# Optimization experiments

Measured on AMD Instinct MI355X. Metric: run time of the kernel, lower is better.

Reference implementation:

```python
import jax, jax.numpy as jnp
import numpy as np

B, T, N, D = 4, 12, 512, 128
L = 4            # max_lag + 1 lag encoders
H = D // 2       # lag-encoder hidden dim
THRESHOLD = 0.1


def setup_inputs() -> dict:
    key = jax.random.key(0)
    ks = jax.random.split(key, 10)
    s = 0.02
    return {
        "x":   jax.random.normal(ks[0], (B, T, N, D), dtype=jnp.float32),
        # lag encoders: Linear(D->H), ReLU, Linear(H->D), stacked over L lags
        "W1":  s * jax.random.normal(ks[1], (L, D, H), dtype=jnp.float32),
        "b1":  jnp.zeros((L, H), dtype=jnp.float32),
        "W2":  s * jax.random.normal(ks[2], (L, H, D), dtype=jnp.float32),
        "b2":  jnp.zeros((L, D), dtype=jnp.float32),
        # causal scorer: Linear(2D->D), ReLU, (Dropout=id in eval), Linear(D->1), Sigmoid
        "Ws1": s * jax.random.normal(ks[3], (2 * D, D), dtype=jnp.float32),
        "bs1": jnp.zeros((D,), dtype=jnp.float32),
        "Ws2": s * jax.random.normal(ks[4], (D, 1), dtype=jnp.float32),
        "bs2": jnp.zeros((1,), dtype=jnp.float32),
    }


def reference(x, W1, b1, W2, b2, Ws1, bs1, Ws2, bs2):
    Tdim = x.shape[1]
    # lagged slices x[:, T-1-lag] for lag in 0..L-1 (all lags active since T > max_lag)
    lags = jnp.stack([x[:, max(0, Tdim - 1 - l)] for l in range(L)], axis=1)  # (B,L,N,D)
    h = jax.nn.relu(jnp.einsum('blnd,ldh->blnh', lags, W1) + b1[None, :, None, :])
    enc = jnp.einsum('blnh,lhd->blnd', h, W2) + b2[None, :, None, :]          # (B,L,N,D)
    agg = enc.mean(axis=1)                                                    # (B,N,D)

    # pairwise causal scorer. cat([src, tgt]) @ Ws1 == src @ Ws1[:D] + tgt @ Ws1[D:],
    # avoiding the explicit (B,N,N,2D) concat.
    src_proj = jnp.einsum('bnd,dk->bnk', agg, Ws1[:D])   # (B,N,D)
    tgt_proj = jnp.einsum('bnd,dk->bnk', agg, Ws1[D:])   # (B,N,D)
    pre = src_proj[:, :, None, :] + tgt_proj[:, None, :, :] + bs1  # (B,N,N,D)
    score = jax.nn.sigmoid(jnp.einsum('bijd,d->bij', jax.nn.relu(pre), Ws2[:, 0]) + bs2[0])

    # threshold sparsification + remove self loops
    adj = jnp.where(score > THRESHOLD, score, 0.0)
    adj = adj * (1.0 - jnp.eye(N, dtype=adj.dtype))

    # multi-hop propagation and global max normalization per batch element
    a2 = jnp.matmul(adj, adj)
    a3 = jnp.matmul(a2, adj)
    enhanced = adj + 0.5 * a2 + 0.25 * a3
    mx = jnp.max(enhanced, axis=(-1, -2), keepdims=True)
    return enhanced / (mx + 1e-8)
```

## Files before the change

kernel.cpp:

```cpp
#include <hip/hip_runtime.h>
#include <math.h>

#define Bn 4
#define Tn 12
#define Nn 512
#define Dn 128
#define Ln 4
#define Hn 64

typedef __attribute__((ext_vector_type(8))) short short8;
typedef __attribute__((ext_vector_type(4))) float f32x4;
typedef _Float16 h2 __attribute__((ext_vector_type(2)));

__device__ __forceinline__ unsigned short f2bf(float f) {
    unsigned int u = __float_as_uint(f);
    unsigned int r = (u + 0x7FFF + ((u >> 16) & 1)) >> 16;
    return (unsigned short)r;
}
__device__ __forceinline__ float bf2f(unsigned short s) {
    return __uint_as_float(((unsigned int)s) << 16);
}
__device__ __forceinline__ float fdot2(h2 a, h2 b, float c) {
#if defined(__has_builtin)
#if __has_builtin(__builtin_amdgcn_fdot2)
    return __builtin_amdgcn_fdot2(a, b, c, false);
#else
    return c + (float)a.x*(float)b.x + (float)a.y*(float)b.y;
#endif
#else
    return c + (float)a.x*(float)b.x + (float)a.y*(float)b.y;
#endif
}

__global__ __launch_bounds__(256) void k_prep(
    const float* __restrict__ W1, const float* __restrict__ W2, const float* __restrict__ Ws1,
    unsigned short* __restrict__ w1p, unsigned short* __restrict__ w2p,
    unsigned short* __restrict__ wsp)
{
    int g = blockIdx.x*256 + threadIdx.x;
    unsigned short tmp[8];
    if (g < 4096) {
        int lag = g >> 10, r = g & 1023;
        int n = r >> 4, k8 = r & 15;
        #pragma unroll
        for (int j = 0; j < 8; ++j) tmp[j] = f2bf(W1[(size_t)(lag*128 + k8*8 + j)*64 + n]);
        *(short8*)(w1p + (size_t)lag*8192 + n*128 + k8*8) = *(const short8*)tmp;
    } else if (g < 8192) {
        int r = g - 4096;
        int n = r >> 5, k8 = r & 31;
        #pragma unroll
        for (int j = 0; j < 8; ++j) tmp[j] = f2bf(W2[(size_t)(k8*8 + j)*128 + n]);
        *(short8*)(w2p + (size_t)n*256 + k8*8) = *(const short8*)tmp;
    } else {
        int r = g - 8192;
        int tgt = r >> 11, r2 = r & 2047;
        int n = r2 >> 4, k8 = r2 & 15;
        #pragma unroll
        for (int j = 0; j < 8; ++j) tmp[j] = f2bf(Ws1[(size_t)(tgt*128 + k8*8 + j)*128 + n]);
        *(short8*)(wsp + (size_t)tgt*16384 + n*128 + k8*8) = *(const short8*)tmp;
    }
}

__global__ __launch_bounds__(256) void k_enc(
    const float* __restrict__ x,  const float* __restrict__ b1,
    const float* __restrict__ b2, const float* __restrict__ bs1,
    const unsigned short* __restrict__ w1p, const unsigned short* __restrict__ w2p,
    const unsigned short* __restrict__ wsp,
    unsigned short* __restrict__ spb, unsigned short* __restrict__ tpb,
    unsigned int* __restrict__ maxslot)
{
    __shared__ __align__(16) unsigned short hA[16*264];
    __shared__ __align__(16) unsigned short xA[16*136];
    __shared__ __align__(16) unsigned short aggA[16*136];
    int tid  = threadIdx.x;
    int bid  = blockIdx.x;
    int wv   = __builtin_amdgcn_readfirstlane(tid >> 6);
    int lane = tid & 63;
    if (bid == 0 && tid < Bn) maxslot[tid] = 0u;

    int r0 = bid * 16;
    int bb = r0 >> 9, n0 = r0 & 511;
    int m = lane & 15, q = lane >> 4;
    int colL = lane & 15, rq = lane >> 4;

    for (int lag = 0; lag < Ln; ++lag) {
        __syncthreads();
        {
            const float4* xs = (const float4*)(x + ((size_t)(bb*Tn + (Tn-1-lag))*Nn + n0)*Dn);
            for (int v = tid; v < 512; v += 256) {
                float4 f = xs[v];
                int row = v >> 5, c4 = v & 31;
                ushort4 o = { f2bf(f.x), f2bf(f.y), f2bf(f.z), f2bf(f.w) };
                *(ushort4*)&xA[row*136 + c4*4] = o;
            }
        }
        __syncthreads();
        f32x4 acc = {0.f,0.f,0.f,0.f};
        #pragma unroll
        for (int ks = 0; ks < 4; ++ks) {
            short8 af = *(const short8*)&xA[m*136 + ks*32 + q*8];
            short8 bg = *(const short8*)(w1p + (size_t)lag*8192 + (wv*16+m)*128 + ks*32 + q*8);
            acc = __builtin_amdgcn_mfma_f32_16x16x32_bf16(af, bg, acc, 0, 0, 0);
        }
        int ncol = wv*16 + colL;
        float bv = b1[lag*Hn + ncol];
        #pragma unroll
        for (int reg = 0; reg < 4; ++reg)
            hA[(rq*4+reg)*264 + lag*64 + ncol] = f2bf(fmaxf(acc[reg] + bv, 0.f));
    }
    __syncthreads();

    #pragma unroll
    for (int ch = 0; ch < 2; ++ch) {
        f32x4 acc = {0.f,0.f,0.f,0.f};
        #pragma unroll
        for (int ks = 0; ks < 8; ++ks) {
            short8 af = *(const short8*)&hA[m*264 + ks*32 + q*8];
            short8 bg = *(const short8*)(w2p + (size_t)(ch*64 + wv*16 + m)*256 + ks*32 + q*8);
            acc = __builtin_amdgcn_mfma_f32_16x16x32_bf16(af, bg, acc, 0, 0, 0);
        }
        int col = ch*64 + wv*16 + colL;
        float b2s = b2[col] + b2[Dn+col] + b2[2*Dn+col] + b2[3*Dn+col];
        #pragma unroll
        for (int reg = 0; reg < 4; ++reg)
            aggA[(rq*4+reg)*136 + col] = f2bf(0.25f*(acc[reg] + b2s));
    }
    __syncthreads();

    #pragma unroll
    for (int tgt = 0; tgt < 2; ++tgt) {
        f32x4 acc[2] = {{0.f,0.f,0.f,0.f},{0.f,0.f,0.f,0.f}};
        #pragma unroll
        for (int ks = 0; ks < 4; ++ks) {
            short8 af = *(const short8*)&aggA[m*136 + ks*32 + q*8];
            #pragma unroll
            for (int nt = 0; nt < 2; ++nt) {
                short8 bg = *(const short8*)(wsp + (size_t)tgt*16384 + (wv*32 + nt*16 + m)*128 + ks*32 + q*8);
                acc[nt] = __builtin_amdgcn_mfma_f32_16x16x32_bf16(af, bg, acc[nt], 0, 0, 0);
            }
        }
        unsigned short* dst = tgt ? tpb : spb;
        #pragma unroll
        for (int nt = 0; nt < 2; ++nt) {
            int n = wv*32 + nt*16 + colL;
            float bv = tgt ? 0.f : bs1[n];
            #pragma unroll
            for (int reg = 0; reg < 4; ++reg) {
                _Float16 hv = (_Float16)(acc[nt][reg] + bv);
                dst[(size_t)(r0 + rq*4 + reg)*Dn + n] = __builtin_bit_cast(unsigned short, hv);
            }
        }
    }
}

__global__ __launch_bounds__(256) void k_score(
    const unsigned short* __restrict__ spb, const unsigned short* __restrict__ tpb,
    const float* __restrict__ Ws2, const float* __restrict__ bs2,
    unsigned short* __restrict__ adj_b, unsigned short* __restrict__ adj_bt)
{
    __shared__ unsigned int spl[64*65];
    __shared__ unsigned int tpl[64*65];
    __shared__ unsigned int wl[64];
    int tid = threadIdx.x;
    int wv = __builtin_amdgcn_readfirstlane(tid >> 6);
    int lane = tid & 63;
    int bz = blockIdx.z;
    int i0b = blockIdx.y * 64, j0b = blockIdx.x * 64;
    const unsigned short* spr = spb + (size_t)bz*Nn*Dn;
    const unsigned short* tpr = tpb + (size_t)bz*Nn*Dn;

    for (int v = tid; v < 1024; v += 256) {
        int row = v >> 4, c = v & 15;
        uint4 gs = *(const uint4*)(spr + (size_t)(i0b+row)*Dn + c*8);
        uint4 gt = *(const uint4*)(tpr + (size_t)(j0b+row)*Dn + c*8);
        spl[row*65 + c*4 + 0] = gs.x; spl[row*65 + c*4 + 1] = gs.y;
        spl[row*65 + c*4 + 2] = gs.z; spl[row*65 + c*4 + 3] = gs.w;
        tpl[row*65 + c*4 + 0] = gt.x; tpl[row*65 + c*4 + 1] = gt.y;
        tpl[row*65 + c*4 + 2] = gt.z; tpl[row*65 + c*4 + 3] = gt.w;
    }
    if (tid < 64) {
        h2 hw = { (_Float16)Ws2[tid*2], (_Float16)Ws2[tid*2+1] };
        wl[tid] = __builtin_bit_cast(unsigned int, hw);
    }
    __syncthreads();

    int iq = lane >> 4, jq = lane & 15;
    int iw = wv*16 + iq*4;
    float acc[4][4] = {};
    #pragma unroll 4
    for (int c = 0; c < 64; ++c) {
        h2 wp = __builtin_bit_cast(h2, wl[c]);
        h2 sh[4], th[4];
        #pragma unroll
        for (int ii = 0; ii < 4; ++ii) sh[ii] = __builtin_bit_cast(h2, spl[(iw+ii)*65 + c]);
        #pragma unroll
        for (int jj = 0; jj < 4; ++jj) th[jj] = __builtin_bit_cast(h2, tpl[(jq*4+jj)*65 + c]);
        #pragma unroll
        for (int ii = 0; ii < 4; ++ii)
            #pragma unroll
            for (int jj = 0; jj < 4; ++jj) {
                h2 r = __builtin_elementwise_max(sh[ii] + th[jj], (h2){(_Float16)0.f,(_Float16)0.f});
                acc[ii][jj] = fdot2(r, wp, acc[ii][jj]);
            }
    }
    float bsv = bs2[0];
    int i0 = i0b + iw;
    int j0 = j0b + jq*4;
    float vals[4][4];
    #pragma unroll
    for (int ii = 0; ii < 4; ++ii) {
        int i = i0 + ii;
        #pragma unroll
        for (int jj = 0; jj < 4; ++jj) {
            float z = acc[ii][jj] + bsv;
            float sc = 1.f/(1.f + __expf(-z));
            int j = j0 + jj;
            vals[ii][jj] = (sc > 0.1f && i != j) ? sc : 0.f;
        }
    }
    size_t base = (size_t)bz << 18;
    #pragma unroll
    for (int ii = 0; ii < 4; ++ii) {
        ushort4 rv = make_ushort4(f2bf(vals[ii][0]), f2bf(vals[ii][1]),
                                  f2bf(vals[ii][2]), f2bf(vals[ii][3]));
        *(ushort4*)(adj_b + base + (size_t)(i0+ii)*Nn + j0) = rv;
    }
    #pragma unroll
    for (int jj = 0; jj < 4; ++jj) {
        ushort4 cv = make_ushort4(f2bf(vals[0][jj]), f2bf(vals[1][jj]),
                                  f2bf(vals[2][jj]), f2bf(vals[3][jj]));
        *(ushort4*)(adj_bt + base + (size_t)(j0+jj)*Nn + i0) = cv;
    }
}

__global__ __launch_bounds__(256) void k_mm1(
    const unsigned short* __restrict__ adj_b, const unsigned short* __restrict__ adj_bt,
    unsigned short* __restrict__ a2b)
{
    __shared__ unsigned short Als[64*72];
    __shared__ unsigned short Bls[64*72];
    int tid = threadIdx.x;
    int wv = __builtin_amdgcn_readfirstlane(tid >> 6);
    int lane = tid & 63;
    int b = blockIdx.z, i0 = blockIdx.y*64, j0 = blockIdx.x*64;
    size_t base = (size_t)b << 18;
    const unsigned short* Ab = adj_b + base;
    const unsigned short* Bb = adj_bt + base;
    int wm = wv >> 1, wn = wv & 1;
    int m = lane & 15, q = lane >> 4;
    int sr = tid >> 2, sc = (tid & 3)*16;
    f32x4 acc[2][2];
    #pragma unroll
    for (int mt = 0; mt < 2; ++mt)
        #pragma unroll
        for (int nt = 0; nt < 2; ++nt) acc[mt][nt] = (f32x4){0.f,0.f,0.f,0.f};
    short8 pa0, pa1, pb0, pb1;
    pa0 = *(const short8*)(Ab + (size_t)(i0+sr)*Nn + sc);
    pa1 = *(const short8*)(Ab + (size_t)(i0+sr)*Nn + sc + 8);
    pb0 = *(const short8*)(Bb + (size_t)(j0+sr)*Nn + sc);
    pb1 = *(const short8*)(Bb + (size_t)(j0+sr)*Nn + sc + 8);
    for (int kt = 0; kt < 8; ++kt) {
        *(short8*)&Als[sr*72 + sc]     = pa0;
        *(short8*)&Als[sr*72 + sc + 8] = pa1;
        *(short8*)&Bls[sr*72 + sc]     = pb0;
        *(short8*)&Bls[sr*72 + sc + 8] = pb1;
        __syncthreads();
        if (kt < 7) {
            int k0 = (kt+1)*64;
            pa0 = *(const short8*)(Ab + (size_t)(i0+sr)*Nn + k0 + sc);
            pa1 = *(const short8*)(Ab + (size_t)(i0+sr)*Nn + k0 + sc + 8);
            pb0 = *(const short8*)(Bb + (size_t)(j0+sr)*Nn + k0 + sc);
            pb1 = *(const short8*)(Bb + (size_t)(j0+sr)*Nn + k0 + sc + 8);
        }
        #pragma unroll
        for (int ks = 0; ks < 2; ++ks) {
            short8 af[2], bg[2];
            #pragma unroll
            for (int mt = 0; mt < 2; ++mt) af[mt] = *(const short8*)&Als[(wm*32+mt*16+m)*72 + ks*32 + q*8];
            #pragma unroll
            for (int nt = 0; nt < 2; ++nt) bg[nt] = *(const short8*)&Bls[(wn*32+nt*16+m)*72 + ks*32 + q*8];
            #pragma unroll
            for (int mt = 0; mt < 2; ++mt)
                #pragma unroll
                for (int nt = 0; nt < 2; ++nt)
                    acc[mt][nt] = __builtin_amdgcn_mfma_f32_16x16x32_bf16(af[mt], bg[nt], acc[mt][nt], 0, 0, 0);
        }
        __syncthreads();
    }
    int col = lane & 15, rq = lane >> 4;
    #pragma unroll
    for (int mt = 0; mt < 2; ++mt)
        #pragma unroll
        for (int nt = 0; nt < 2; ++nt)
            #pragma unroll
            for (int reg = 0; reg < 4; ++reg) {
                int i = i0 + wm*32 + mt*16 + rq*4 + reg;
                int j = j0 + wn*32 + nt*16 + col;
                a2b[base + (size_t)i*Nn + j] = f2bf(acc[mt][nt][reg]);
            }
}

__global__ __launch_bounds__(256) void k_mm2(
    const unsigned short* __restrict__ adj_b, const unsigned short* __restrict__ adj_bt,
    const unsigned short* __restrict__ a2b,
    float* __restrict__ out, unsigned int* __restrict__ maxslot)
{
    __shared__ unsigned short Als[64*72];
    __shared__ unsigned short Bls[64*72];
    __shared__ float red[4];
    int tid = threadIdx.x;
    int wv = __builtin_amdgcn_readfirstlane(tid >> 6);
    int lane = tid & 63;
    int b = blockIdx.z, i0 = blockIdx.y*64, j0 = blockIdx.x*64;
    size_t base = (size_t)b << 18;
    const unsigned short* Ab = a2b + base;
    const unsigned short* Bb = adj_bt + base;
    int wm = wv >> 1, wn = wv & 1;
    int m = lane & 15, q = lane >> 4;
    int sr = tid >> 2, sc = (tid & 3)*16;
    f32x4 acc[2][2];
    #pragma unroll
    for (int mt = 0; mt < 2; ++mt)
        #pragma unroll
        for (int nt = 0; nt < 2; ++nt) acc[mt][nt] = (f32x4){0.f,0.f,0.f,0.f};
    short8 pa0, pa1, pb0, pb1;
    pa0 = *(const short8*)(Ab + (size_t)(i0+sr)*Nn + sc);
    pa1 = *(const short8*)(Ab + (size_t)(i0+sr)*Nn + sc + 8);
    pb0 = *(const short8*)(Bb + (size_t)(j0+sr)*Nn + sc);
    pb1 = *(const short8*)(Bb + (size_t)(j0+sr)*Nn + sc + 8);
    for (int kt = 0; kt < 8; ++kt) {
        *(short8*)&Als[sr*72 + sc]     = pa0;
        *(short8*)&Als[sr*72 + sc + 8] = pa1;
        *(short8*)&Bls[sr*72 + sc]     = pb0;
        *(short8*)&Bls[sr*72 + sc + 8] = pb1;
        __syncthreads();
        if (kt < 7) {
            int k0 = (kt+1)*64;
            pa0 = *(const short8*)(Ab + (size_t)(i0+sr)*Nn + k0 + sc);
            pa1 = *(const short8*)(Ab + (size_t)(i0+sr)*Nn + k0 + sc + 8);
            pb0 = *(const short8*)(Bb + (size_t)(j0+sr)*Nn + k0 + sc);
            pb1 = *(const short8*)(Bb + (size_t)(j0+sr)*Nn + k0 + sc + 8);
        }
        #pragma unroll
        for (int ks = 0; ks < 2; ++ks) {
            short8 af[2], bg[2];
            #pragma unroll
            for (int mt = 0; mt < 2; ++mt) af[mt] = *(const short8*)&Als[(wm*32+mt*16+m)*72 + ks*32 + q*8];
            #pragma unroll
            for (int nt = 0; nt < 2; ++nt) bg[nt] = *(const short8*)&Bls[(wn*32+nt*16+m)*72 + ks*32 + q*8];
            #pragma unroll
            for (int mt = 0; mt < 2; ++mt)
                #pragma unroll
                for (int nt = 0; nt < 2; ++nt)
                    acc[mt][nt] = __builtin_amdgcn_mfma_f32_16x16x32_bf16(af[mt], bg[nt], acc[mt][nt], 0, 0, 0);
        }
        __syncthreads();
    }
    int col = lane & 15, rq = lane >> 4;
    float lmax = 0.f;
    const unsigned short* adjp = adj_b + base;
    #pragma unroll
    for (int mt = 0; mt < 2; ++mt)
        #pragma unroll
        for (int nt = 0; nt < 2; ++nt)
            #pragma unroll
            for (int reg = 0; reg < 4; ++reg) {
                int i = i0 + wm*32 + mt*16 + rq*4 + reg;
                int j = j0 + wn*32 + nt*16 + col;
                size_t off = (size_t)i*Nn + j;
                float e = bf2f(adjp[off]) + 0.5f*bf2f(Ab[off]) + 0.25f*acc[mt][nt][reg];
                out[base + off] = e;
                lmax = fmaxf(lmax, e);
            }
    #pragma unroll
    for (int s = 1; s < 64; s <<= 1) lmax = fmaxf(lmax, __shfl_xor(lmax, s, 64));
    if (lane == 0) red[wv] = lmax;
    __syncthreads();
    if (tid == 0) {
        float mx = fmaxf(fmaxf(red[0], red[1]), fmaxf(red[2], red[3]));
        atomicMax(maxslot + b, __float_as_uint(mx));
    }
}

__global__ __launch_bounds__(256) void k_norm(float* __restrict__ out,
                                              const unsigned int* __restrict__ maxslot)
{
    int idx = blockIdx.x*256 + threadIdx.x;
    int b = idx >> 16;
    float m = __uint_as_float(maxslot[b]);
    float inv = 1.f/(m + 1e-8f);
    float4* p = (float4*)out + idx;
    float4 v = *p;
    v.x *= inv; v.y *= inv; v.z *= inv; v.w *= inv;
    *p = v;
}

extern "C" void kernel_launch(void* const* d_in, const int* in_sizes, int n_in,
                              void* d_out, int out_size, void* d_ws, size_t ws_size,
                              hipStream_t stream) {
    const float* x   = (const float*)d_in[0];
    const float* W1  = (const float*)d_in[1];
    const float* b1  = (const float*)d_in[2];
    const float* W2  = (const float*)d_in[3];
    const float* b2  = (const float*)d_in[4];
    const float* Ws1 = (const float*)d_in[5];
    const float* bs1 = (const float*)d_in[6];
    const float* Ws2 = (const float*)d_in[7];
    const float* bs2 = (const float*)d_in[8];
    float* out = (float*)d_out;

    unsigned char* wsb = (unsigned char*)d_ws;
    unsigned short* spb    = (unsigned short*)(wsb);
    unsigned short* tpb    = (unsigned short*)(wsb + (512u<<10));
    unsigned short* adj_b  = (unsigned short*)(wsb + (1024u<<10));
    unsigned short* adj_bt = (unsigned short*)(wsb + (3072u<<10));
    unsigned short* a2b    = (unsigned short*)(wsb + (5120u<<10));
    unsigned int*   maxslot= (unsigned int*)(wsb + (7168u<<10));
    unsigned short* w1p    = (unsigned short*)(wsb + (7172u<<10));
    unsigned short* w2p    = (unsigned short*)(wsb + (7236u<<10));
    unsigned short* wsp    = (unsigned short*)(wsb + (7300u<<10));

    k_prep <<<dim3(48),       256, 0, stream>>>(W1, W2, Ws1, w1p, w2p, wsp);
    k_enc  <<<dim3(128),      256, 0, stream>>>(x, b1, b2, bs1, w1p, w2p, wsp, spb, tpb, maxslot);
    k_score<<<dim3(8, 8, Bn), 256, 0, stream>>>(spb, tpb, Ws2, bs2, adj_b, adj_bt);
    k_mm1  <<<dim3(8, 8, Bn), 256, 0, stream>>>(adj_b, adj_bt, a2b);
    k_mm2  <<<dim3(8, 8, Bn), 256, 0, stream>>>(adj_b, adj_bt, a2b, out, maxslot);
    k_norm <<<dim3(1024),     256, 0, stream>>>(out, maxslot);
}
```

Before: 118.6 us.

## Fuse the two adjacency matmuls into one row-block kernel keeping A² in LDS

Replaces the separate A·A and A²·A kernels with one kernel. Each 512-thread block owns 16 full rows of one batch, computes those rows of A² into shared memory, then multiplies them by A again and writes the enhanced output plus the block max. This removes the A² round trip through global memory and one kernel launch. B operands are streamed straight from global memory into registers with a 4-deep prefetch instead of LDS tiles. The grid shrinks to 128 blocks, which may leave many CUs idle, and every block rereads the whole transposed adjacency twice.

Result: slower. 132.7 us (+11.9%).

```diff
diff --git a/kernel.cpp b/kernel.cpp
--- a/kernel.cpp
+++ b/kernel.cpp
@@ -233,152 +233,108 @@
     }
 }
 
-__global__ __launch_bounds__(256) void k_mm1(
+__global__ __launch_bounds__(512) void k_prop(
     const unsigned short* __restrict__ adj_b, const unsigned short* __restrict__ adj_bt,
-    unsigned short* __restrict__ a2b)
-{
-    __shared__ unsigned short Als[64*72];
-    __shared__ unsigned short Bls[64*72];
+    float* __restrict__ out, unsigned int* __restrict__ maxslot)
+{
+    __shared__ __align__(16) unsigned short adjA[16*520];
+    __shared__ __align__(16) unsigned short a2ls[16*520];
+    __shared__ float red[8];
     int tid = threadIdx.x;
     int wv = __builtin_amdgcn_readfirstlane(tid >> 6);
     int lane = tid & 63;
-    int b = blockIdx.z, i0 = blockIdx.y*64, j0 = blockIdx.x*64;
-    size_t base = (size_t)b << 18;
+    int i0 = blockIdx.x * 16, bz = blockIdx.y;
+    size_t base = (size_t)bz << 18;
     const unsigned short* Ab = adj_b + base;
     const unsigned short* Bb = adj_bt + base;
-    int wm = wv >> 1, wn = wv & 1;
+
+    for (int v = tid; v < 1024; v += 512) {
+        int row = v >> 6, c = v & 63;
+        *(short8*)&adjA[row*520 + c*8] = *(const short8*)(Ab + (size_t)(i0+row)*Nn + c*8);
+    }
+    __syncthreads();
+
     int m = lane & 15, q = lane >> 4;
-    int sr = tid >> 2, sc = (tid & 3)*16;
-    f32x4 acc[2][2];
-    #pragma unroll
-    for (int mt = 0; mt < 2; ++mt)
-        #pragma unroll
-        for (int nt = 0; nt < 2; ++nt) acc[mt][nt] = (f32x4){0.f,0.f,0.f,0.f};
-    short8 pa0, pa1, pb0, pb1;
-    pa0 = *(const short8*)(Ab + (size_t)(i0+sr)*Nn + sc);
-    pa1 = *(const short8*)(Ab + (size_t)(i0+sr)*Nn + sc + 8);
-    pb0 = *(const short8*)(Bb + (size_t)(j0+sr)*Nn + sc);
-    pb1 = *(const short8*)(Bb + (size_t)(j0+sr)*Nn + sc + 8);
-    for (int kt = 0; kt < 8; ++kt) {
-        *(short8*)&Als[sr*72 + sc]     = pa0;
-        *(short8*)&Als[sr*72 + sc + 8] = pa1;
-        *(short8*)&Bls[sr*72 + sc]     = pb0;
-        *(short8*)&Bls[sr*72 + sc + 8] = pb1;
-        __syncthreads();
-        if (kt < 7) {
-            int k0 = (kt+1)*64;
-            pa0 = *(const short8*)(Ab + (size_t)(i0+sr)*Nn + k0 + sc);
-            pa1 = *(const short8*)(Ab + (size_t)(i0+sr)*Nn + k0 + sc + 8);
-            pb0 = *(const short8*)(Bb + (size_t)(j0+sr)*Nn + k0 + sc);
-            pb1 = *(const short8*)(Bb + (size_t)(j0+sr)*Nn + k0 + sc + 8);
-        }
-        #pragma unroll
-        for (int ks = 0; ks < 2; ++ks) {
-            short8 af[2], bg[2];
-            #pragma unroll
-            for (int mt = 0; mt < 2; ++mt) af[mt] = *(const short8*)&Als[(wm*32+mt*16+m)*72 + ks*32 + q*8];
-            #pragma unroll
-            for (int nt = 0; nt < 2; ++nt) bg[nt] = *(const short8*)&Bls[(wn*32+nt*16+m)*72 + ks*32 + q*8];
-            #pragma unroll
-            for (int mt = 0; mt < 2; ++mt)
-                #pragma unroll
-                for (int nt = 0; nt < 2; ++nt)
-                    acc[mt][nt] = __builtin_amdgcn_mfma_f32_16x16x32_bf16(af[mt], bg[nt], acc[mt][nt], 0, 0, 0);
-        }
-        __syncthreads();
-    }
-    int col = lane & 15, rq = lane >> 4;
-    #pragma unroll
-    for (int mt = 0; mt < 2; ++mt)
-        #pragma unroll
-        for (int nt = 0; nt < 2; ++nt)
-            #pragma unroll
-            for (int reg = 0; reg < 4; ++reg) {
-                int i = i0 + wm*32 + mt*16 + rq*4 + reg;
-                int j = j0 + wn*32 + nt*16 + col;
-                a2b[base + (size_t)i*Nn + j] = f2bf(acc[mt][nt][reg]);
-            }
-}
-
-__global__ __launch_bounds__(256) void k_mm2(
-    const unsigned short* __restrict__ adj_b, const unsigned short* __restrict__ adj_bt,
-    const unsigned short* __restrict__ a2b,
-    float* __restrict__ out, unsigned int* __restrict__ maxslot)
-{
-    __shared__ unsigned short Als[64*72];
-    __shared__ unsigned short Bls[64*72];
-    __shared__ float red[4];
-    int tid = threadIdx.x;
-    int wv = __builtin_amdgcn_readfirstlane(tid >> 6);
-    int lane = tid & 63;
-    int b = blockIdx.z, i0 = blockIdx.y*64, j0 = blockIdx.x*64;
-    size_t base = (size_t)b << 18;
-    const unsigned short* Ab = a2b + base;
-    const unsigned short* Bb = adj_bt + base;
-    int wm = wv >> 1, wn = wv & 1;
-    int m = lane & 15, q = lane >> 4;
-    int sr = tid >> 2, sc = (tid & 3)*16;
-    f32x4 acc[2][2];
-    #pragma unroll
-    for (int mt = 0; mt < 2; ++mt)
-        #pragma unroll
-        for (int nt = 0; nt < 2; ++nt) acc[mt][nt] = (f32x4){0.f,0.f,0.f,0.f};
-    short8 pa0, pa1, pb0, pb1;
-    pa0 = *(const short8*)(Ab + (size_t)(i0+sr)*Nn + sc);
-    pa1 = *(const short8*)(Ab + (size_t)(i0+sr)*Nn + sc + 8);
-    pb0 = *(const short8*)(Bb + (size_t)(j0+sr)*Nn + sc);
-    pb1 = *(const short8*)(Bb + (size_t)(j0+sr)*Nn + sc + 8);
-    for (int kt = 0; kt < 8; ++kt) {
-        *(short8*)&Als[sr*72 + sc]     = pa0;
-        *(short8*)&Als[sr*72 + sc + 8] = pa1;
-        *(short8*)&Bls[sr*72 + sc]     = pb0;
-        *(short8*)&Bls[sr*72 + sc + 8] = pb1;
-        __syncthreads();
-        if (kt < 7) {
-            int k0 = (kt+1)*64;
-            pa0 = *(const short8*)(Ab + (size_t)(i0+sr)*Nn + k0 + sc);
-            pa1 = *(const short8*)(Ab + (size_t)(i0+sr)*Nn + k0 + sc + 8);
-            pb0 = *(const short8*)(Bb + (size_t)(j0+sr)*Nn + k0 + sc);
-            pb1 = *(const short8*)(Bb + (size_t)(j0+sr)*Nn + k0 + sc + 8);
-        }
-        #pragma unroll
-        for (int ks = 0; ks < 2; ++ks) {
-            short8 af[2], bg[2];
-            #pragma unroll
-            for (int mt = 0; mt < 2; ++mt) af[mt] = *(const short8*)&Als[(wm*32+mt*16+m)*72 + ks*32 + q*8];
-            #pragma unroll
-            for (int nt = 0; nt < 2; ++nt) bg[nt] = *(const short8*)&Bls[(wn*32+nt*16+m)*72 + ks*32 + q*8];
-            #pragma unroll
-            for (int mt = 0; mt < 2; ++mt)
-                #pragma unroll
-                for (int nt = 0; nt < 2; ++nt)
-                    acc[mt][nt] = __builtin_amdgcn_mfma_f32_16x16x32_bf16(af[mt], bg[nt], acc[mt][nt], 0, 0, 0);
-        }
-        __syncthreads();
-    }
-    int col = lane & 15, rq = lane >> 4;
+    int colL = m, rq = q;
+    const unsigned short* Bw = Bb + (size_t)(wv*64 + m)*Nn + q*8;
+
+    f32x4 acc[4];
+    short8 bgbuf[4][4];
+    #pragma unroll
+    for (int pk = 0; pk < 4; ++pk)
+        #pragma unroll
+        for (int jt = 0; jt < 4; ++jt)
+            bgbuf[pk][jt] = *(const short8*)(Bw + jt*16*Nn + pk*32);
+    #pragma unroll
+    for (int jt = 0; jt < 4; ++jt) acc[jt] = (f32x4){0.f,0.f,0.f,0.f};
+    #pragma unroll
+    for (int ks = 0; ks < 16; ++ks) {
+        short8 af = *(const short8*)&adjA[m*520 + ks*32 + q*8];
+        short8 cur[4];
+        #pragma unroll
+        for (int jt = 0; jt < 4; ++jt) cur[jt] = bgbuf[ks & 3][jt];
+        if (ks < 12) {
+            #pragma unroll
+            for (int jt = 0; jt < 4; ++jt)
+                bgbuf[ks & 3][jt] = *(const short8*)(Bw + jt*16*Nn + (ks+4)*32);
+        }
+        #pragma unroll
+        for (int jt = 0; jt < 4; ++jt)
+            acc[jt] = __builtin_amdgcn_mfma_f32_16x16x32_bf16(af, cur[jt], acc[jt], 0, 0, 0);
+    }
+    #pragma unroll
+    for (int jt = 0; jt < 4; ++jt) {
+        int j = wv*64 + jt*16 + colL;
+        #pragma unroll
+        for (int reg = 0; reg < 4; ++reg)
+            a2ls[(rq*4+reg)*520 + j] = f2bf(acc[jt][reg]);
+    }
+    __syncthreads();
+
+    #pragma unroll
+    for (int pk = 0; pk < 4; ++pk)
+        #pragma unroll
+        for (int jt = 0; jt < 4; ++jt)
+            bgbuf[pk][jt] = *(const short8*)(Bw + jt*16*Nn + pk*32);
+    #pragma unroll
+    for (int jt = 0; jt < 4; ++jt) acc[jt] = (f32x4){0.f,0.f,0.f,0.f};
+    #pragma unroll
+    for (int ks = 0; ks < 16; ++ks) {
+        short8 af = *(const short8*)&a2ls[m*520 + ks*32 + q*8];
+        short8 cur[4];
+        #pragma unroll
+        for (int jt = 0; jt < 4; ++jt) cur[jt] = bgbuf[ks & 3][jt];
+        if (ks < 12) {
+            #pragma unroll
+            for (int jt = 0; jt < 4; ++jt)
+                bgbuf[ks & 3][jt] = *(const short8*)(Bw + jt*16*Nn + (ks+4)*32);
+        }
+        #pragma unroll
+        for (int jt = 0; jt < 4; ++jt)
+            acc[jt] = __builtin_amdgcn_mfma_f32_16x16x32_bf16(af, cur[jt], acc[jt], 0, 0, 0);
+    }
+
     float lmax = 0.f;
-    const unsigned short* adjp = adj_b + base;
-    #pragma unroll
-    for (int mt = 0; mt < 2; ++mt)
-        #pragma unroll
-        for (int nt = 0; nt < 2; ++nt)
-            #pragma unroll
-            for (int reg = 0; reg < 4; ++reg) {
-                int i = i0 + wm*32 + mt*16 + rq*4 + reg;
-                int j = j0 + wn*32 + nt*16 + col;
-                size_t off = (size_t)i*Nn + j;
-                float e = bf2f(adjp[off]) + 0.5f*bf2f(Ab[off]) + 0.25f*acc[mt][nt][reg];
-                out[base + off] = e;
-                lmax = fmaxf(lmax, e);
-            }
+    #pragma unroll
+    for (int jt = 0; jt < 4; ++jt) {
+        int j = wv*64 + jt*16 + colL;
+        #pragma unroll
+        for (int reg = 0; reg < 4; ++reg) {
+            int r = rq*4 + reg;
+            float e = bf2f(adjA[r*520 + j]) + 0.5f*bf2f(a2ls[r*520 + j]) + 0.25f*acc[jt][reg];
+            out[base + (size_t)(i0+r)*Nn + j] = e;
+            lmax = fmaxf(lmax, e);
+        }
+    }
     #pragma unroll
     for (int s = 1; s < 64; s <<= 1) lmax = fmaxf(lmax, __shfl_xor(lmax, s, 64));
     if (lane == 0) red[wv] = lmax;
     __syncthreads();
     if (tid == 0) {
-        float mx = fmaxf(fmaxf(red[0], red[1]), fmaxf(red[2], red[3]));
-        atomicMax(maxslot + b, __float_as_uint(mx));
+        float mx = red[0];
+        #pragma unroll
+        for (int w = 1; w < 8; ++w) mx = fmaxf(mx, red[w]);
+        atomicMax(maxslot + bz, __float_as_uint(mx));
     }
 }
 
@@ -414,7 +370,6 @@
     unsigned short* tpb    = (unsigned short*)(wsb + (512u<<10));
     unsigned short* adj_b  = (unsigned short*)(wsb + (1024u<<10));
     unsigned short* adj_bt = (unsigned short*)(wsb + (3072u<<10));
-    unsigned short* a2b    = (unsigned short*)(wsb + (5120u<<10));
     unsigned int*   maxslot= (unsigned int*)(wsb + (7168u<<10));
     unsigned short* w1p    = (unsigned short*)(wsb + (7172u<<10));
     unsigned short* w2p    = (unsigned short*)(wsb + (7236u<<10));
@@ -423,7 +378,6 @@
     k_prep <<<dim3(48),       256, 0, stream>>>(W1, W2, Ws1, w1p, w2p, wsp);
     k_enc  <<<dim3(128),      256, 0, stream>>>(x, b1, b2, bs1, w1p, w2p, wsp, spb, tpb, maxslot);
     k_score<<<dim3(8, 8, Bn), 256, 0, stream>>>(spb, tpb, Ws2, bs2, adj_b, adj_bt);
-    k_mm1  <<<dim3(8, 8, Bn), 256, 0, stream>>>(adj_b, adj_bt, a2b);
-    k_mm2  <<<dim3(8, 8, Bn), 256, 0, stream>>>(adj_b, adj_bt, a2b, out, maxslot);
+    k_prop <<<dim3(32, Bn),   512, 0, stream>>>(adj_b, adj_bt, out, maxslot);
     k_norm <<<dim3(1024),     256, 0, stream>>>(out, maxslot);
 }
```

## Widen encoder kernel to 8 waves and load all lag slices at once

Applied to the files above, without the earlier changes.

The encoder kernel now runs with 512 threads (8 wavefronts) per block instead of 256. All four lagged x slices are loaded into shared memory in one pass, and each wave pair handles one lag, replacing the serial per-lag loop and its two barriers per iteration. The second and third GEMM stages split output columns and source/target across the 8 waves rather than looping. This exposes more parallelism and memory-level concurrency in a 128-block kernel, at the cost of more shared memory and register pressure per block.

New measurement: 117.1 us. No clear change (-1.2%).

```diff
diff --git a/kernel.cpp b/kernel.cpp
--- a/kernel.cpp
+++ b/kernel.cpp
@@ -61,7 +61,7 @@
     }
 }
 
-__global__ __launch_bounds__(256) void k_enc(
+__global__ __launch_bounds__(512) void k_enc(
     const float* __restrict__ x,  const float* __restrict__ b1,
     const float* __restrict__ b2, const float* __restrict__ bs1,
     const unsigned short* __restrict__ w1p, const unsigned short* __restrict__ w2p,
@@ -69,8 +69,8 @@
     unsigned short* __restrict__ spb, unsigned short* __restrict__ tpb,
     unsigned int* __restrict__ maxslot)
 {
+    __shared__ __align__(16) unsigned short xAll[4][16*136];
     __shared__ __align__(16) unsigned short hA[16*264];
-    __shared__ __align__(16) unsigned short xA[16*136];
     __shared__ __align__(16) unsigned short aggA[16*136];
     int tid  = threadIdx.x;
     int bid  = blockIdx.x;
@@ -83,43 +83,48 @@
     int m = lane & 15, q = lane >> 4;
     int colL = lane & 15, rq = lane >> 4;
 
-    for (int lag = 0; lag < Ln; ++lag) {
-        __syncthreads();
-        {
-            const float4* xs = (const float4*)(x + ((size_t)(bb*Tn + (Tn-1-lag))*Nn + n0)*Dn);
-            for (int v = tid; v < 512; v += 256) {
-                float4 f = xs[v];
-                int row = v >> 5, c4 = v & 31;
-                ushort4 o = { f2bf(f.x), f2bf(f.y), f2bf(f.z), f2bf(f.w) };
-                *(ushort4*)&xA[row*136 + c4*4] = o;
-            }
-        }
-        __syncthreads();
-        f32x4 acc = {0.f,0.f,0.f,0.f};
+    for (int v = tid; v < 2048; v += 512) {
+        int lag = v >> 9, r = v & 511;
+        int row = r >> 5, c4 = r & 31;
+        const float4* xs = (const float4*)(x + ((size_t)(bb*Tn + (Tn-1-lag))*Nn + n0)*Dn);
+        float4 f = xs[row*32 + c4];
+        ushort4 o = { f2bf(f.x), f2bf(f.y), f2bf(f.z), f2bf(f.w) };
+        *(ushort4*)&xAll[lag][row*136 + c4*4] = o;
+    }
+    __syncthreads();
+
+    {
+        int lag = wv >> 1, hf = wv & 1;
+        f32x4 acc[2] = {{0.f,0.f,0.f,0.f},{0.f,0.f,0.f,0.f}};
         #pragma unroll
         for (int ks = 0; ks < 4; ++ks) {
-            short8 af = *(const short8*)&xA[m*136 + ks*32 + q*8];
-            short8 bg = *(const short8*)(w1p + (size_t)lag*8192 + (wv*16+m)*128 + ks*32 + q*8);
-            acc = __builtin_amdgcn_mfma_f32_16x16x32_bf16(af, bg, acc, 0, 0, 0);
-        }
-        int ncol = wv*16 + colL;
-        float bv = b1[lag*Hn + ncol];
-        #pragma unroll
-        for (int reg = 0; reg < 4; ++reg)
-            hA[(rq*4+reg)*264 + lag*64 + ncol] = f2bf(fmaxf(acc[reg] + bv, 0.f));
+            short8 af = *(const short8*)&xAll[lag][m*136 + ks*32 + q*8];
+            #pragma unroll
+            for (int nt = 0; nt < 2; ++nt) {
+                short8 bg = *(const short8*)(w1p + (size_t)lag*8192 + (hf*32 + nt*16 + m)*128 + ks*32 + q*8);
+                acc[nt] = __builtin_amdgcn_mfma_f32_16x16x32_bf16(af, bg, acc[nt], 0, 0, 0);
+            }
+        }
+        #pragma unroll
+        for (int nt = 0; nt < 2; ++nt) {
+            int ncol = hf*32 + nt*16 + colL;
+            float bv = b1[lag*Hn + ncol];
+            #pragma unroll
+            for (int reg = 0; reg < 4; ++reg)
+                hA[(rq*4+reg)*264 + lag*64 + ncol] = f2bf(fmaxf(acc[nt][reg] + bv, 0.f));
+        }
     }
     __syncthreads();
 
-    #pragma unroll
-    for (int ch = 0; ch < 2; ++ch) {
+    {
         f32x4 acc = {0.f,0.f,0.f,0.f};
         #pragma unroll
         for (int ks = 0; ks < 8; ++ks) {
             short8 af = *(const short8*)&hA[m*264 + ks*32 + q*8];
-            short8 bg = *(const short8*)(w2p + (size_t)(ch*64 + wv*16 + m)*256 + ks*32 + q*8);
+            short8 bg = *(const short8*)(w2p + (size_t)(wv*16 + m)*256 + ks*32 + q*8);
             acc = __builtin_amdgcn_mfma_f32_16x16x32_bf16(af, bg, acc, 0, 0, 0);
         }
-        int col = ch*64 + wv*16 + colL;
+        int col = wv*16 + colL;
         float b2s = b2[col] + b2[Dn+col] + b2[2*Dn+col] + b2[3*Dn+col];
         #pragma unroll
         for (int reg = 0; reg < 4; ++reg)
@@ -127,22 +132,22 @@
     }
     __syncthreads();
 
-    #pragma unroll
-    for (int tgt = 0; tgt < 2; ++tgt) {
+    {
+        int tgt = wv >> 2, wv4 = wv & 3;
         f32x4 acc[2] = {{0.f,0.f,0.f,0.f},{0.f,0.f,0.f,0.f}};
         #pragma unroll
         for (int ks = 0; ks < 4; ++ks) {
             short8 af = *(const short8*)&aggA[m*136 + ks*32 + q*8];
             #pragma unroll
             for (int nt = 0; nt < 2; ++nt) {
-                short8 bg = *(const short8*)(wsp + (size_t)tgt*16384 + (wv*32 + nt*16 + m)*128 + ks*32 + q*8);
+                short8 bg = *(const short8*)(wsp + (size_t)tgt*16384 + (wv4*32 + nt*16 + m)*128 + ks*32 + q*8);
                 acc[nt] = __builtin_amdgcn_mfma_f32_16x16x32_bf16(af, bg, acc[nt], 0, 0, 0);
             }
         }
         unsigned short* dst = tgt ? tpb : spb;
         #pragma unroll
         for (int nt = 0; nt < 2; ++nt) {
-            int n = wv*32 + nt*16 + colL;
+            int n = wv4*32 + nt*16 + colL;
             float bv = tgt ? 0.f : bs1[n];
             #pragma unroll
             for (int reg = 0; reg < 4; ++reg) {
@@ -421,7 +426,7 @@
     unsigned short* wsp    = (unsigned short*)(wsb + (7300u<<10));
 
     k_prep <<<dim3(48),       256, 0, stream>>>(W1, W2, Ws1, w1p, w2p, wsp);
-    k_enc  <<<dim3(128),      256, 0, stream>>>(x, b1, b2, bs1, w1p, w2p, wsp, spb, tpb, maxslot);
+    k_enc  <<<dim3(128),      512, 0, stream>>>(x, b1, b2, bs1, w1p, w2p, wsp, spb, tpb, maxslot);
     k_score<<<dim3(8, 8, Bn), 256, 0, stream>>>(spb, tpb, Ws2, bs2, adj_b, adj_bt);
     k_mm1  <<<dim3(8, 8, Bn), 256, 0, stream>>>(adj_b, adj_bt, a2b);
     k_mm2  <<<dim3(8, 8, Bn), 256, 0, stream>>>(adj_b, adj_bt, a2b, out, maxslot);
```
